# Kernel optimization log

Measured on AMD Instinct MI355X. Metric: run time of the kernel, lower is better.

The kernel has to match this reference:

```python
import jax, jax.numpy as jnp
import numpy as np

DIM = 4096
NH = 32       # query heads
NKV = 8       # kv heads
HD = DIM // NH  # 128
B = 1
S = 2048
ROPE_BASE = 10000.0


def rope_tables(seq_len, head_dim, base=ROPE_BASE):
    inv_freq = 1.0 / base ** (jnp.arange(0, head_dim, 2, dtype=jnp.float32) / head_dim)
    t = jnp.arange(seq_len, dtype=jnp.float32)
    freqs = jnp.einsum('i,j->ij', t, inv_freq)          # [S, HD/2]
    emb = jnp.concatenate([freqs, freqs], axis=-1)      # [S, HD]
    return jnp.cos(emb), jnp.sin(emb)


def apply_rope(x, cos, sin):
    # x: [B, H, S, HD]; matches torch apply_rotary_emb (chunk halves)
    x1, x2 = jnp.split(x, 2, axis=-1)
    d = x1.shape[-1]
    c = cos[None, None, :, :d]
    s = sin[None, None, :, :d]
    return jnp.concatenate([x1 * c - x2 * s, x2 * c + x1 * s], axis=-1)


def setup_inputs() -> dict:
    key = jax.random.key(0)
    k0, k1, k2, k3, k4 = jax.random.split(key, 5)
    sc = 0.02  # typical init scale for stable softmax
    return {
        'x': jax.random.normal(k0, (B, S, DIM), jnp.float32),
        'wq': jax.random.normal(k1, (DIM, NH * HD), jnp.float32) * sc,
        'wk': jax.random.normal(k2, (DIM, NKV * HD), jnp.float32) * sc,
        'wv': jax.random.normal(k3, (DIM, NKV * HD), jnp.float32) * sc,
        'wo': jax.random.normal(k4, (NH * HD, DIM), jnp.float32) * sc,
        'mask': jnp.ones((1,), jnp.bool_),  # presence triggers is_causal=True in torch SDPA path
    }


def reference(x, wq, wk, wv, wo, mask):
    Bsz, Sl, _ = x.shape
    n_rep = NH // NKV
    q = (x @ wq).reshape(Bsz, Sl, NH, HD).transpose(0, 2, 1, 3)    # [B,NH,S,HD]
    k = (x @ wk).reshape(Bsz, Sl, NKV, HD).transpose(0, 2, 1, 3)   # [B,NKV,S,HD]
    v = (x @ wv).reshape(Bsz, Sl, NKV, HD).transpose(0, 2, 1, 3)
    cos, sin = rope_tables(Sl, HD)
    q = apply_rope(q, cos, sin)
    k = apply_rope(k, cos, sin)
    # GQA without repeat_interleave: group query heads per kv head
    qg = q.reshape(Bsz, NKV, n_rep, Sl, HD)
    scale = HD ** -0.5
    scores = jnp.einsum('bgrqd,bgkd->bgrqk', qg, k) * scale        # [B,NKV,n_rep,S,S]
    causal = jnp.tril(jnp.ones((Sl, Sl), dtype=bool))
    scores = jnp.where(causal[None, None, None], scores, jnp.finfo(scores.dtype).min)
    attn = jax.nn.softmax(scores, axis=-1)
    out = jnp.einsum('bgrqk,bgkd->bgrqd', attn, v)                 # [B,NKV,n_rep,S,HD]
    out = out.reshape(Bsz, NH, Sl, HD).transpose(0, 2, 1, 3).reshape(Bsz, Sl, NH * HD)
    return out @ wo
```

## Files before the change

kernel.cpp:

```cpp
#include <hip/hip_runtime.h>
#include <hip/hip_bf16.h>
#include <cstdint>
#include <cmath>

#define DIM 4096
#define NH 32
#define NKV 8
#define HD 128
#define S_LEN 2048
#define KVD (NKV * HD)
#define QS 6144
#define SCALE 0.08838834764831845f

typedef __attribute__((ext_vector_type(4))) float f32x4;
typedef __attribute__((ext_vector_type(8))) short short8;

__device__ __forceinline__ short f2bf(float f) {
  union { float f; uint32_t u; } v; v.f = f;
  uint32_t u = v.u;
  u += 0x7fffu + ((u >> 16) & 1u);
  return (short)(u >> 16);
}
__device__ __forceinline__ float bf2f(short b) {
  union { uint32_t u; float f; } v; v.u = ((uint32_t)(uint16_t)b) << 16;
  return v.f;
}

__device__ __forceinline__ void async16(const void* g, void* l) {
  __builtin_amdgcn_global_load_lds(
      (__attribute__((address_space(1))) void*)(g),
      (__attribute__((address_space(3))) void*)(l), 16, 0, 0);
}


__global__ void rope_tables_k(float* __restrict__ ct, float* __restrict__ st) {
  const int i = blockIdx.x * blockDim.x + threadIdx.x;
  if (i >= S_LEN * 64) return;
  const int s = i >> 6, d = i & 63;
  const float inv = powf(10000.0f, -(float)(2 * d) / 128.0f);
  const float fr = (float)s * inv;
  ct[i] = cosf(fr);
  st[i] = sinf(fr);
}

__global__ void cast_f32_bf16_k(const float* __restrict__ in, short* __restrict__ out, int n4) {
  const int i = blockIdx.x * blockDim.x + threadIdx.x;
  if (i >= n4) return;
  const float4 v = ((const float4*)in)[i];
  short4 o;
  o.x = f2bf(v.x); o.y = f2bf(v.y); o.z = f2bf(v.z); o.w = f2bf(v.w);
  ((short4*)out)[i] = o;
}

__global__ void transpose_cast_k(const float* __restrict__ wsrc, short* __restrict__ wt,
                                 int K, int N) {
  __shared__ float tile[32][33];
  const int tx = threadIdx.x, ty = threadIdx.y;
  const int c0 = blockIdx.x * 32, r0 = blockIdx.y * 32;
#pragma unroll
  for (int j = 0; j < 4; ++j)
    tile[ty + j * 8][tx] = wsrc[(size_t)(r0 + ty + j * 8) * N + c0 + tx];
  __syncthreads();
#pragma unroll
  for (int j = 0; j < 4; ++j)
    wt[(size_t)(c0 + ty + j * 8) * K + r0 + tx] = f2bf(tile[tx][ty + j * 8]);
}

__global__ void transpose_bf16_k(const short* __restrict__ in, short* __restrict__ out,
                                 int R, int C, int ldi) {
  __shared__ short tile[32][33];
  const int tx = threadIdx.x, ty = threadIdx.y;
  const int c0 = blockIdx.x * 32, r0 = blockIdx.y * 32;
#pragma unroll
  for (int j = 0; j < 4; ++j)
    tile[ty + j * 8][tx] = in[(size_t)(r0 + ty + j * 8) * ldi + c0 + tx];
  __syncthreads();
#pragma unroll
  for (int j = 0; j < 4; ++j)
    out[(size_t)(c0 + ty + j * 8) * R + r0 + tx] = tile[tx][ty + j * 8];
}

__global__ void rope_apply_k(short* __restrict__ xq, int ld, const float* __restrict__ ct,
                             const float* __restrict__ st, int nheads) {
  const int i = blockIdx.x * blockDim.x + threadIdx.x;
  const int total = S_LEN * nheads * 64;
  if (i >= total) return;
  const int d = i & 63;
  const int t = i >> 6;
  const int hh = t % nheads;
  const int s = t / nheads;
  short* p = xq + (size_t)s * ld + hh * HD + d;
  const float x1 = bf2f(p[0]);
  const float x2 = bf2f(p[64]);
  const float c = ct[(s << 6) + d];
  const float sn = st[(s << 6) + d];
  p[0]  = f2bf(x1 * c - x2 * sn);
  p[64] = f2bf(x2 * c + x1 * sn);
}


#define PH3_SYNC(VM)                                             \
  asm volatile("s_waitcnt vmcnt(" #VM ")" ::: "memory");         \
  __builtin_amdgcn_s_barrier();                                  \
  asm volatile("s_waitcnt lgkmcnt(0)" ::: "memory");             \
  __builtin_amdgcn_sched_barrier(0);                             \
  __builtin_amdgcn_s_setprio(1)

#define PH3_END()                                                \
  __builtin_amdgcn_s_setprio(0);                                 \
  __builtin_amdgcn_sched_barrier(0);                             \
  __builtin_amdgcn_s_barrier()

__global__ __launch_bounds__(512, 2) void gemm192_k(
    const short* __restrict__ A, const short* __restrict__ BT,
    short* __restrict__ C, int M, int N, int K) {
  __shared__ __attribute__((aligned(16))) short ldsA[2][256 * 64];
  __shared__ __attribute__((aligned(16))) short ldsB[2][192 * 64];
  const int tid = threadIdx.x;
  const int l = tid & 63, w = tid >> 6;
  const int wrM = w >> 1, wcN = w & 1;
  const int lrow = l & 15, lg = l >> 4;
  const int cofs[2] = {(lg ^ (lrow & 7)) << 3, ((4 + lg) ^ (lrow & 7)) << 3};
  (void)M;

  int bid = blockIdx.x;
  const int cpx = gridDim.x >> 3;
  bid = (bid & 7) * cpx + (bid >> 3);
  const int ntn = N / 192;
  const int m0 = (bid / ntn) << 8;
  const int n0 = (bid % ntn) * 192;

  auto stage = [&](int tau) {
    const int k0 = tau << 6;
    short* bd = &ldsB[tau & 1][0];
    short* ad = &ldsA[tau & 1][0];
#pragma unroll
    for (int it = 0; it < 3; ++it) {
      const int e = it * 512 + tid;
      const int row = e >> 3;
      const int js = (e & 7) ^ (row & 7);
      async16(BT + (size_t)(n0 + row) * K + k0 + js * 8, bd + e * 8);
    }
#pragma unroll
    for (int it = 0; it < 4; ++it) {
      const int e = it * 512 + tid;
      const int row = e >> 3;
      const int js = (e & 7) ^ (row & 7);
      async16(A + (size_t)(m0 + row) * K + k0 + js * 8, ad + e * 8);
    }
  };
  auto rdA = [&](short8 (&dst)[4][2], int b) {
    const short* p = &ldsA[b][0];
#pragma unroll
    for (int mi = 0; mi < 4; ++mi) {
      const int row = wrM * 64 + mi * 16 + lrow;
#pragma unroll
      for (int kk = 0; kk < 2; ++kk)
        dst[mi][kk] = *(const short8*)(p + row * 64 + cofs[kk]);
    }
  };
  auto rdB = [&](short8 (&dst)[2][2], int b, int pr) {
    const short* p = &ldsB[b][0];
#pragma unroll
    for (int ni = 0; ni < 2; ++ni) {
      const int row = wcN * 96 + pr * 32 + ni * 16 + lrow;
#pragma unroll
      for (int kk = 0; kk < 2; ++kk)
        dst[ni][kk] = *(const short8*)(p + row * 64 + cofs[kk]);
    }
  };

  f32x4 acc[4][6] = {};
  auto third = [&](short8 (&Af)[4][2], int pr, short8 (&Bf)[2][2]) {
#pragma unroll
    for (int kk = 0; kk < 2; ++kk)
#pragma unroll
      for (int mi = 0; mi < 4; ++mi)
#pragma unroll
        for (int ni = 0; ni < 2; ++ni)
          acc[mi][pr * 2 + ni] = __builtin_amdgcn_mfma_f32_16x16x32_bf16(
              Af[mi][kk], Bf[ni][kk], acc[mi][pr * 2 + ni], 0, 0, 0);
  };

  short8 Aa[4][2], Ab[4][2], B0f[2][2], B1f[2][2], B2f[2][2];

  stage(0); stage(1);
  asm volatile("s_waitcnt vmcnt(7)" ::: "memory");
  __builtin_amdgcn_s_barrier();
  rdB(B0f, 0, 0);
  rdA(Aa, 0);

  const int KT = K >> 6;
  for (int u = 0; u < (KT - 2) / 2; ++u) {
    const int e = 2 * u;
    rdB(B1f, 0, 1); rdB(B2f, 0, 2);
    PH3_SYNC(7);  third(Aa, 0, B0f); PH3_END();
    stage(e + 2);
    PH3_SYNC(7);  third(Aa, 1, B1f); PH3_END();
    rdB(B0f, 1, 0); rdA(Ab, 1);
    PH3_SYNC(7);  third(Aa, 2, B2f); PH3_END();
    rdB(B1f, 1, 1); rdB(B2f, 1, 2);
    PH3_SYNC(7);  third(Ab, 0, B0f); PH3_END();
    stage(e + 3);
    PH3_SYNC(7);  third(Ab, 1, B1f); PH3_END();
    rdB(B0f, 0, 0); rdA(Aa, 0);
    PH3_SYNC(7);  third(Ab, 2, B2f); PH3_END();
  }
  rdB(B1f, 0, 1); rdB(B2f, 0, 2);
  PH3_SYNC(7);  third(Aa, 0, B0f); PH3_END();
  PH3_SYNC(0);  third(Aa, 1, B1f); PH3_END();
  rdB(B0f, 1, 0); rdA(Ab, 1);
  PH3_SYNC(0);  third(Aa, 2, B2f); PH3_END();
  rdB(B1f, 1, 1); rdB(B2f, 1, 2);
  PH3_SYNC(0);  third(Ab, 0, B0f); PH3_END();
  PH3_SYNC(0);  third(Ab, 1, B1f); PH3_END();
  PH3_SYNC(0);  third(Ab, 2, B2f); PH3_END();

  const int orow0 = m0 + wrM * 64 + lg * 4;
  const int ocol0 = n0 + wcN * 96 + lrow;
#pragma unroll
  for (int mi = 0; mi < 4; ++mi)
#pragma unroll
    for (int n = 0; n < 6; ++n)
#pragma unroll
      for (int r = 0; r < 4; ++r)
        C[(size_t)(orow0 + mi * 16 + r) * N + (ocol0 + n * 16)] = f2bf(acc[mi][n][r]);
}


template <int BM, int NBUF, int OUT_BF16>
__global__ __launch_bounds__(512, 2) void gemm_p(
    const short* __restrict__ A, const short* __restrict__ BT,
    void* __restrict__ Cv, int M, int N, int K) {
  constexpr int TILE = (BM + 256) * 64;
  constexpr int LA = BM / 64;
  constexpr int NP = BM / 64;
  __shared__ __attribute__((aligned(16))) short lds[NBUF][TILE];

  const int tid = threadIdx.x;
  const int w = tid >> 6, l = tid & 63;
  const int wr = w >> 2, wc = w & 3;
  const int lrow = l & 15, lg = l >> 4;

  int bid = blockIdx.x;
  const int cpx = gridDim.x >> 3;
  bid = (bid & 7) * cpx + (bid >> 3);
  const int ntn = N >> 8;
  const int m0 = (bid / ntn) * BM;
  const int n0 = (bid % ntn) << 8;

  auto stage = [&](int kt, int buf) {
    const int k0 = kt << 6;
    short* dst = &lds[buf][0];
#pragma unroll
    for (int it = 0; it < LA; ++it) {
      const int e = it * 512 + tid;
      const int row = e >> 3, j = e & 7;
      const int jsrc = j ^ (row & 7);
      async16(A + (size_t)(m0 + row) * K + k0 + jsrc * 8, dst + e * 8);
    }
#pragma unroll
    for (int it = 0; it < 4; ++it) {
      const int e = it * 512 + tid;
      const int row = e >> 3, j = e & 7;
      const int jsrc = j ^ (row & 7);
      async16(BT + (size_t)(n0 + row) * K + k0 + jsrc * 8, dst + BM * 64 + e * 8);
    }
  };

  auto vwait = [&](int J) {
    if constexpr (BM == 256) {
      if (J >= 1) asm volatile("s_waitcnt vmcnt(8)" ::: "memory");
      else        asm volatile("s_waitcnt vmcnt(0)" ::: "memory");
    } else {
      if (J >= 2)      asm volatile("s_waitcnt vmcnt(12)" ::: "memory");
      else if (J == 1) asm volatile("s_waitcnt vmcnt(6)" ::: "memory");
      else             asm volatile("s_waitcnt vmcnt(0)" ::: "memory");
    }
  };

  f32x4 acc[NP * 2][4] = {};

  const int KT = K >> 6;
#pragma unroll
  for (int t = 0; t < NBUF; ++t) stage(t, t);
  vwait(NBUF - 1);
  __builtin_amdgcn_s_barrier();

  for (int kt = 0; kt < KT; ++kt) {
    const int buf = kt % NBUF;
    const short* Ah = &lds[buf][0];
    const short* Bh = &lds[buf][BM * 64];
    short8 bfrag[2][4];

#pragma unroll
    for (int p = 0; p < NP; ++p) {
      short8 afrag[2][2];
#pragma unroll
      for (int mi = 0; mi < 2; ++mi) {
        const int row = wr * (BM / 2) + (p * 2 + mi) * 16 + lrow;
#pragma unroll
        for (int kk = 0; kk < 2; ++kk)
          afrag[mi][kk] =
              *(const short8*)(Ah + row * 64 + (((kk * 4 + lg) ^ (row & 7)) << 3));
      }
      if (p == 0) {
#pragma unroll
        for (int n = 0; n < 4; ++n) {
          const int row = wc * 64 + n * 16 + lrow;
#pragma unroll
          for (int kk = 0; kk < 2; ++kk)
            bfrag[kk][n] =
                *(const short8*)(Bh + row * 64 + (((kk * 4 + lg) ^ (row & 7)) << 3));
        }
      }
      __builtin_amdgcn_s_barrier();
      asm volatile("s_waitcnt lgkmcnt(0)" ::: "memory");
      __builtin_amdgcn_s_setprio(1);
#pragma unroll
      for (int kk = 0; kk < 2; ++kk)
#pragma unroll
        for (int mi = 0; mi < 2; ++mi)
#pragma unroll
          for (int n = 0; n < 4; ++n)
            acc[p * 2 + mi][n] = __builtin_amdgcn_mfma_f32_16x16x32_bf16(
                afrag[mi][kk], bfrag[kk][n], acc[p * 2 + mi][n], 0, 0, 0);
      __builtin_amdgcn_s_setprio(0);
      __builtin_amdgcn_s_barrier();
    }
    if (kt + 1 < KT) {
      const int nst = kt + NBUF;
      if (nst < KT) stage(nst, buf);
      const int J = (nst < KT ? nst : KT - 1) - (kt + 1);
      vwait(J);
      __builtin_amdgcn_s_barrier();
    }
  }

  const int orow0 = m0 + wr * (BM / 2) + lg * 4;
  const int ocol0 = n0 + wc * 64 + lrow;
#pragma unroll
  for (int m = 0; m < NP * 2; ++m)
#pragma unroll
    for (int n = 0; n < 4; ++n)
#pragma unroll
      for (int r = 0; r < 4; ++r) {
        const size_t idx = (size_t)(orow0 + m * 16 + r) * N + (ocol0 + n * 16);
        if (OUT_BF16)
          ((short*)Cv)[idx] = f2bf(acc[m][n][r]);
        else
          ((float*)Cv)[idx] = acc[m][n][r];
      }
}


__global__ __launch_bounds__(256, 3) void attn_k(
    const short* __restrict__ Q, const short* __restrict__ Kc,
    const short* __restrict__ VTg, short* __restrict__ O) {
  __shared__ __attribute__((aligned(16))) short Ks[2][64 * 128];
  __shared__ __attribute__((aligned(16))) short Vt[2][128 * 64];
  __shared__ __attribute__((aligned(16))) short Ps[4][32 * 64];

  const int tid = threadIdx.x;
  const int w = tid >> 6, l = tid & 63;
  const int lrow = l & 15, lg = l >> 4;

  int b = blockIdx.x, h, qt;
  if (b < 256) { h = b >> 3; qt = 15 - (b & 7); }
  else { b -= 256; h = b >> 3; qt = b & 7; }
  const int kvh = h >> 2;
  const int qb0 = qt * 128;
  const int qrow0 = qb0 + w * 32;
  const int nkt = 2 * qt + 2;

  short8 qf[2][4];
#pragma unroll
  for (int nq = 0; nq < 2; ++nq) {
    const short* qp = Q + (size_t)(qrow0 + nq * 16 + lrow) * QS + h * HD;
#pragma unroll
    for (int c = 0; c < 4; ++c) qf[nq][c] = *(const short8*)(qp + c * 32 + lg * 8);
  }

  f32x4 o_acc[2][8] = {};
  float m[2] = {-INFINITY, -INFINITY};
  float lsum[2] = {0.f, 0.f};

  auto stage = [&](int kb, int buf) {
    short* kd = Ks[buf];
    short* vd = Vt[buf];
#pragma unroll
    for (int it = 0; it < 4; ++it) {
      const int e = it * 256 + tid;
      const int row = e >> 4, j = e & 15;
      const int jsrc = (j & 8) | ((j ^ row) & 7);
      async16(Kc + (size_t)(kb + row) * QS + kvh * HD + jsrc * 8, kd + e * 8);
    }
#pragma unroll
    for (int it = 0; it < 4; ++it) {
      const int e = it * 256 + tid;
      const int d = e >> 3, j = e & 7;
      const int jsrc = (j ^ d) & 7;
      async16(VTg + (size_t)(kvh * HD + d) * S_LEN + kb + jsrc * 8, vd + e * 8);
    }
  };

  stage(0, 0);
  int cur = 0;

  for (int kt = 0; kt < nkt; ++kt) {
    __syncthreads();
    if (kt + 1 < nkt) stage((kt + 1) * 64, cur ^ 1);
    const int kb = kt * 64;

    if (kb <= qrow0 + 31) {
      const char* ks = (const char*)Ks[cur];
      const char* vt = (const char*)Vt[cur];
      char* psb = (char*)Ps[w];

      f32x4 stq[4][2] = {};
#pragma unroll
      for (int c = 0; c < 4; ++c) {
#pragma unroll
        for (int mk = 0; mk < 4; ++mk) {
          const short8 kf = *(const short8*)(
              ks + (mk * 16 + lrow) * 256 + (((c * 4 + lg) ^ (lrow & 7)) << 4));
          stq[mk][0] = __builtin_amdgcn_mfma_f32_16x16x32_bf16(kf, qf[0][c], stq[mk][0], 0, 0, 0);
          stq[mk][1] = __builtin_amdgcn_mfma_f32_16x16x32_bf16(kf, qf[1][c], stq[mk][1], 0, 0, 0);
        }
      }

      const bool needmask = (kb + 63 > qrow0);
#pragma unroll
      for (int mk = 0; mk < 4; ++mk)
#pragma unroll
        for (int nq = 0; nq < 2; ++nq)
#pragma unroll
          for (int r = 0; r < 4; ++r) {
            float v = stq[mk][nq][r] * SCALE;
            if (needmask && (kb + mk * 16 + lg * 4 + r > qrow0 + nq * 16 + lrow))
              v = -INFINITY;
            stq[mk][nq][r] = v;
          }

      float vmax[2];
#pragma unroll
      for (int nq = 0; nq < 2; ++nq) {
        float v = stq[0][nq][0];
#pragma unroll
        for (int mk = 0; mk < 4; ++mk)
#pragma unroll
          for (int r = 0; r < 4; ++r) v = fmaxf(v, stq[mk][nq][r]);
        v = fmaxf(v, __shfl_xor(v, 16));
        v = fmaxf(v, __shfl_xor(v, 32));
        vmax[nq] = v;
      }

      const int small = (vmax[0] <= m[0] + 8.0f) && (vmax[1] <= m[1] + 8.0f);
      if (!__all(small)) {
        float al[2];
#pragma unroll
        for (int nq = 0; nq < 2; ++nq) {
          const float mn = fmaxf(m[nq], vmax[nq]);
          al[nq] = __expf(m[nq] - mn);
          m[nq] = mn;
          lsum[nq] *= al[nq];
        }
#pragma unroll
        for (int mmq = 0; mmq < 2; ++mmq)
#pragma unroll
          for (int r = 0; r < 4; ++r) {
            const float a = __shfl(al[mmq], lg * 4 + r);
#pragma unroll
            for (int d = 0; d < 8; ++d) o_acc[mmq][d][r] *= a;
          }
      }

      float rs[2] = {0.f, 0.f};
#pragma unroll
      for (int nq = 0; nq < 2; ++nq) {
#pragma unroll
        for (int mk = 0; mk < 4; ++mk) {
          const float p0 = __expf(stq[mk][nq][0] - m[nq]);
          const float p1 = __expf(stq[mk][nq][1] - m[nq]);
          const float p2 = __expf(stq[mk][nq][2] - m[nq]);
          const float p3 = __expf(stq[mk][nq][3] - m[nq]);
          rs[nq] += (p0 + p1) + (p2 + p3);
          __hip_bfloat16 b0 = __float2bfloat16(p0), b1 = __float2bfloat16(p1);
          __hip_bfloat16 b2 = __float2bfloat16(p2), b3 = __float2bfloat16(p3);
          short4 pk;
          pk.x = *(short*)&b0; pk.y = *(short*)&b1; pk.z = *(short*)&b2; pk.w = *(short*)&b3;
          const int q = nq * 16 + lrow;
          *(short4*)(psb + q * 128 + ((mk * 32 + lg * 8) ^ ((q & 7) << 4))) = pk;
        }
        float r2 = rs[nq];
        r2 += __shfl_xor(r2, 16);
        r2 += __shfl_xor(r2, 32);
        lsum[nq] += r2;
      }

#pragma unroll
      for (int cc = 0; cc < 2; ++cc) {
        const int chunk = ((cc * 4 + lg) ^ (lrow & 7)) << 4;
        const short8 pa0 = *(const short8*)(psb + lrow * 128 + chunk);
        const short8 pa1 = *(const short8*)(psb + (16 + lrow) * 128 + chunk);
#pragma unroll
        for (int d = 0; d < 8; ++d) {
          const short8 vf = *(const short8*)(vt + (d * 16 + lrow) * 128 + chunk);
          o_acc[0][d] = __builtin_amdgcn_mfma_f32_16x16x32_bf16(pa0, vf, o_acc[0][d], 0, 0, 0);
          o_acc[1][d] = __builtin_amdgcn_mfma_f32_16x16x32_bf16(pa1, vf, o_acc[1][d], 0, 0, 0);
        }
      }
    }
    cur ^= 1;
  }

  float linv[2] = {1.0f / lsum[0], 1.0f / lsum[1]};
#pragma unroll
  for (int mmq = 0; mmq < 2; ++mmq)
#pragma unroll
    for (int r = 0; r < 4; ++r) {
      const float li = __shfl(linv[mmq], lg * 4 + r);
      short* op = O + (size_t)(qrow0 + mmq * 16 + lg * 4 + r) * DIM + h * HD;
#pragma unroll
      for (int d = 0; d < 8; ++d)
        op[d * 16 + lrow] = f2bf(o_acc[mmq][d][r] * li);
    }
}


extern "C" void kernel_launch(void* const* d_in, const int* in_sizes, int n_in,
                              void* d_out, int out_size, void* d_ws, size_t ws_size,
                              hipStream_t stream) {
  const float* x  = (const float*)d_in[0];
  const float* wq = (const float*)d_in[1];
  const float* wk = (const float*)d_in[2];
  const float* wv = (const float*)d_in[3];
  const float* wo = (const float*)d_in[4];
  float* out = (float*)d_out;
  (void)in_sizes; (void)n_in; (void)out_size; (void)ws_size;

  char* ws = (char*)d_ws;
  size_t off = 0;
  auto alloc = [&](size_t bytes) -> void* {
    void* p = ws + off;
    off += (bytes + 255) & ~(size_t)255;
    return p;
  };
  short* xb     = (short*)alloc((size_t)S_LEN * DIM * 2);
  short* wqkvT  = (short*)alloc((size_t)QS * DIM * 2);
  short* woT    = (short*)alloc((size_t)DIM * DIM * 2);
  short* qkv    = (short*)alloc((size_t)S_LEN * QS * 2);
  short* vtg    = (short*)alloc((size_t)KVD * S_LEN * 2);
  short* ao     = (short*)alloc((size_t)S_LEN * DIM * 2);
  float* ct     = (float*)alloc((size_t)S_LEN * 64 * 4);
  float* st     = (float*)alloc((size_t)S_LEN * 64 * 4);

  rope_tables_k<<<(S_LEN * 64) / 256, 256, 0, stream>>>(ct, st);
  cast_f32_bf16_k<<<(S_LEN * DIM / 4) / 256, 256, 0, stream>>>(x, xb, S_LEN * DIM / 4);
  transpose_cast_k<<<dim3(DIM / 32, DIM / 32), dim3(32, 8), 0, stream>>>(wq, wqkvT, DIM, DIM);
  transpose_cast_k<<<dim3(KVD / 32, DIM / 32), dim3(32, 8), 0, stream>>>(
      wk, wqkvT + (size_t)4096 * DIM, DIM, KVD);
  transpose_cast_k<<<dim3(KVD / 32, DIM / 32), dim3(32, 8), 0, stream>>>(
      wv, wqkvT + (size_t)5120 * DIM, DIM, KVD);
  transpose_cast_k<<<dim3(DIM / 32, DIM / 32), dim3(32, 8), 0, stream>>>(wo, woT, DIM, DIM);

  gemm192_k<<<dim3((S_LEN / 256) * (QS / 192)), 512, 0, stream>>>(
      xb, wqkvT, qkv, S_LEN, QS, DIM);

  rope_apply_k<<<(S_LEN * 40 * 64) / 256, 256, 0, stream>>>(qkv, QS, ct, st, 40);

  transpose_bf16_k<<<dim3(KVD / 32, S_LEN / 32), dim3(32, 8), 0, stream>>>(
      qkv + 5120, vtg, S_LEN, KVD, QS);

  attn_k<<<dim3(512), 256, 0, stream>>>(qkv, qkv + 4096, vtg, ao);

  gemm_p<128, 3, 0><<<dim3((S_LEN / 128) * (DIM / 256)), 512, 0, stream>>>(
      ao, woT, out, S_LEN, DIM, DIM);
}
```

Measured before the change: 354.1 us.

## Rewrite output GEMM with double-buffered register-prefetch pipeline and partial lgkm waits

Replaces the generic triple-buffered gemm_p for the output projection with a dedicated double-buffered kernel. It prefetches A and B fragments into registers ahead of the MFMA phases, splits each k-tile into two halves, and issues global staging inside barrier-protected phases. In the QKV GEMM it also relaxes the lgkmcnt waits to partial counts and moves the stage calls inside the synced phases. The aim is to overlap LDS reads and global loads with MFMA work and cut stall time, at the cost of more register pressure and subtle wait-count correctness requirements.

```diff
diff --git a/kernel.cpp b/kernel.cpp
--- a/kernel.cpp
+++ b/kernel.cpp
@@ -98,18 +98,18 @@
   p[64] = f2bf(x2 * c + x1 * sn);
 }
 
-
-#define PH3_SYNC(VM)                                             \
+#define SYNC2(VM, LG)                                            \
   asm volatile("s_waitcnt vmcnt(" #VM ")" ::: "memory");         \
   __builtin_amdgcn_s_barrier();                                  \
-  asm volatile("s_waitcnt lgkmcnt(0)" ::: "memory");             \
+  asm volatile("s_waitcnt lgkmcnt(" #LG ")" ::: "memory");       \
   __builtin_amdgcn_sched_barrier(0);                             \
   __builtin_amdgcn_s_setprio(1)
 
-#define PH3_END()                                                \
+#define PH_END()                                                 \
   __builtin_amdgcn_s_setprio(0);                                 \
   __builtin_amdgcn_sched_barrier(0);                             \
   __builtin_amdgcn_s_barrier()
+
 
 __global__ __launch_bounds__(512, 2) void gemm192_k(
     const short* __restrict__ A, const short* __restrict__ BT,
@@ -194,27 +194,25 @@
   for (int u = 0; u < (KT - 2) / 2; ++u) {
     const int e = 2 * u;
     rdB(B1f, 0, 1); rdB(B2f, 0, 2);
-    PH3_SYNC(7);  third(Aa, 0, B0f); PH3_END();
-    stage(e + 2);
-    PH3_SYNC(7);  third(Aa, 1, B1f); PH3_END();
+    SYNC2(7, 8);  third(Aa, 0, B0f); PH_END();
+    SYNC2(0, 0);  stage(e + 2); third(Aa, 1, B1f); PH_END();
     rdB(B0f, 1, 0); rdA(Ab, 1);
-    PH3_SYNC(7);  third(Aa, 2, B2f); PH3_END();
+    SYNC2(7, 12); third(Aa, 2, B2f); PH_END();
     rdB(B1f, 1, 1); rdB(B2f, 1, 2);
-    PH3_SYNC(7);  third(Ab, 0, B0f); PH3_END();
-    stage(e + 3);
-    PH3_SYNC(7);  third(Ab, 1, B1f); PH3_END();
+    SYNC2(7, 8);  third(Ab, 0, B0f); PH_END();
+    SYNC2(0, 0);  stage(e + 3); third(Ab, 1, B1f); PH_END();
     rdB(B0f, 0, 0); rdA(Aa, 0);
-    PH3_SYNC(7);  third(Ab, 2, B2f); PH3_END();
+    SYNC2(7, 12); third(Ab, 2, B2f); PH_END();
   }
   rdB(B1f, 0, 1); rdB(B2f, 0, 2);
-  PH3_SYNC(7);  third(Aa, 0, B0f); PH3_END();
-  PH3_SYNC(0);  third(Aa, 1, B1f); PH3_END();
+  SYNC2(7, 8);  third(Aa, 0, B0f); PH_END();
+  SYNC2(0, 0);  third(Aa, 1, B1f); PH_END();
   rdB(B0f, 1, 0); rdA(Ab, 1);
-  PH3_SYNC(0);  third(Aa, 2, B2f); PH3_END();
+  SYNC2(0, 12); third(Aa, 2, B2f); PH_END();
   rdB(B1f, 1, 1); rdB(B2f, 1, 2);
-  PH3_SYNC(0);  third(Ab, 0, B0f); PH3_END();
-  PH3_SYNC(0);  third(Ab, 1, B1f); PH3_END();
-  PH3_SYNC(0);  third(Ab, 2, B2f); PH3_END();
+  SYNC2(0, 8);  third(Ab, 0, B0f); PH_END();
+  SYNC2(0, 0);  third(Ab, 1, B1f); PH_END();
+  SYNC2(0, 0);  third(Ab, 2, B2f); PH_END();
 
   const int orow0 = m0 + wrM * 64 + lg * 4;
   const int ocol0 = n0 + wcN * 96 + lrow;
@@ -228,129 +226,113 @@
 }
 
 
-template <int BM, int NBUF, int OUT_BF16>
-__global__ __launch_bounds__(512, 2) void gemm_p(
+__global__ __launch_bounds__(512, 2) void gemm_wo2_k(
     const short* __restrict__ A, const short* __restrict__ BT,
-    void* __restrict__ Cv, int M, int N, int K) {
-  constexpr int TILE = (BM + 256) * 64;
-  constexpr int LA = BM / 64;
-  constexpr int NP = BM / 64;
-  __shared__ __attribute__((aligned(16))) short lds[NBUF][TILE];
-
+    float* __restrict__ C, int M, int N, int K) {
+  __shared__ __attribute__((aligned(16))) short ldsA[2][128 * 64];
+  __shared__ __attribute__((aligned(16))) short ldsB[2][256 * 64];
   const int tid = threadIdx.x;
-  const int w = tid >> 6, l = tid & 63;
-  const int wr = w >> 2, wc = w & 3;
+  const int l = tid & 63, w = tid >> 6;
+  const int wrM = w >> 2, wcN = w & 3;
   const int lrow = l & 15, lg = l >> 4;
+  const int cofs[2] = {(lg ^ (lrow & 7)) << 3, ((4 + lg) ^ (lrow & 7)) << 3};
+  (void)M;
 
   int bid = blockIdx.x;
   const int cpx = gridDim.x >> 3;
   bid = (bid & 7) * cpx + (bid >> 3);
   const int ntn = N >> 8;
-  const int m0 = (bid / ntn) * BM;
+  const int m0 = (bid / ntn) << 7;
   const int n0 = (bid % ntn) << 8;
 
-  auto stage = [&](int kt, int buf) {
-    const int k0 = kt << 6;
-    short* dst = &lds[buf][0];
-#pragma unroll
-    for (int it = 0; it < LA; ++it) {
+  auto stage = [&](int tau) {
+    const int k0 = tau << 6;
+    short* ad = &ldsA[tau & 1][0];
+    short* bd = &ldsB[tau & 1][0];
+#pragma unroll
+    for (int it = 0; it < 2; ++it) {
       const int e = it * 512 + tid;
-      const int row = e >> 3, j = e & 7;
-      const int jsrc = j ^ (row & 7);
-      async16(A + (size_t)(m0 + row) * K + k0 + jsrc * 8, dst + e * 8);
+      const int row = e >> 3;
+      const int js = (e & 7) ^ (row & 7);
+      async16(A + (size_t)(m0 + row) * K + k0 + js * 8, ad + e * 8);
     }
 #pragma unroll
     for (int it = 0; it < 4; ++it) {
       const int e = it * 512 + tid;
-      const int row = e >> 3, j = e & 7;
-      const int jsrc = j ^ (row & 7);
-      async16(BT + (size_t)(n0 + row) * K + k0 + jsrc * 8, dst + BM * 64 + e * 8);
-    }
-  };
-
-  auto vwait = [&](int J) {
-    if constexpr (BM == 256) {
-      if (J >= 1) asm volatile("s_waitcnt vmcnt(8)" ::: "memory");
-      else        asm volatile("s_waitcnt vmcnt(0)" ::: "memory");
-    } else {
-      if (J >= 2)      asm volatile("s_waitcnt vmcnt(12)" ::: "memory");
-      else if (J == 1) asm volatile("s_waitcnt vmcnt(6)" ::: "memory");
-      else             asm volatile("s_waitcnt vmcnt(0)" ::: "memory");
-    }
-  };
-
-  f32x4 acc[NP * 2][4] = {};
+      const int row = e >> 3;
+      const int js = (e & 7) ^ (row & 7);
+      async16(BT + (size_t)(n0 + row) * K + k0 + js * 8, bd + e * 8);
+    }
+  };
+  auto rdA = [&](short8 (&dst)[4][2], int b) {
+    const short* p = &ldsA[b][0];
+#pragma unroll
+    for (int mi = 0; mi < 4; ++mi) {
+      const int row = wrM * 64 + mi * 16 + lrow;
+#pragma unroll
+      for (int kk = 0; kk < 2; ++kk)
+        dst[mi][kk] = *(const short8*)(p + row * 64 + cofs[kk]);
+    }
+  };
+  auto rdB = [&](short8 (&dst)[2][2], int b, int h) {
+    const short* p = &ldsB[b][0];
+#pragma unroll
+    for (int ni = 0; ni < 2; ++ni) {
+      const int row = wcN * 64 + h * 32 + ni * 16 + lrow;
+#pragma unroll
+      for (int kk = 0; kk < 2; ++kk)
+        dst[ni][kk] = *(const short8*)(p + row * 64 + cofs[kk]);
+    }
+  };
+
+  f32x4 acc[4][4] = {};
+  auto half = [&](short8 (&Af)[4][2], int h, short8 (&Bf)[2][2]) {
+#pragma unroll
+    for (int kk = 0; kk < 2; ++kk)
+#pragma unroll
+      for (int mi = 0; mi < 4; ++mi)
+#pragma unroll
+        for (int ni = 0; ni < 2; ++ni)
+          acc[mi][h * 2 + ni] = __builtin_amdgcn_mfma_f32_16x16x32_bf16(
+              Af[mi][kk], Bf[ni][kk], acc[mi][h * 2 + ni], 0, 0, 0);
+  };
+
+  short8 Aa[4][2], Ab[4][2], H0[2][2], H1[2][2];
+
+  stage(0); stage(1);
+  asm volatile("s_waitcnt vmcnt(6)" ::: "memory");
+  __builtin_amdgcn_s_barrier();
+  rdA(Aa, 0); rdB(H0, 0, 0);
 
   const int KT = K >> 6;
-#pragma unroll
-  for (int t = 0; t < NBUF; ++t) stage(t, t);
-  vwait(NBUF - 1);
-  __builtin_amdgcn_s_barrier();
-
-  for (int kt = 0; kt < KT; ++kt) {
-    const int buf = kt % NBUF;
-    const short* Ah = &lds[buf][0];
-    const short* Bh = &lds[buf][BM * 64];
-    short8 bfrag[2][4];
-
-#pragma unroll
-    for (int p = 0; p < NP; ++p) {
-      short8 afrag[2][2];
-#pragma unroll
-      for (int mi = 0; mi < 2; ++mi) {
-        const int row = wr * (BM / 2) + (p * 2 + mi) * 16 + lrow;
-#pragma unroll
-        for (int kk = 0; kk < 2; ++kk)
-          afrag[mi][kk] =
-              *(const short8*)(Ah + row * 64 + (((kk * 4 + lg) ^ (row & 7)) << 3));
-      }
-      if (p == 0) {
-#pragma unroll
-        for (int n = 0; n < 4; ++n) {
-          const int row = wc * 64 + n * 16 + lrow;
-#pragma unroll
-          for (int kk = 0; kk < 2; ++kk)
-            bfrag[kk][n] =
-                *(const short8*)(Bh + row * 64 + (((kk * 4 + lg) ^ (row & 7)) << 3));
-        }
-      }
-      __builtin_amdgcn_s_barrier();
-      asm volatile("s_waitcnt lgkmcnt(0)" ::: "memory");
-      __builtin_amdgcn_s_setprio(1);
-#pragma unroll
-      for (int kk = 0; kk < 2; ++kk)
-#pragma unroll
-        for (int mi = 0; mi < 2; ++mi)
-#pragma unroll
-          for (int n = 0; n < 4; ++n)
-            acc[p * 2 + mi][n] = __builtin_amdgcn_mfma_f32_16x16x32_bf16(
-                afrag[mi][kk], bfrag[kk][n], acc[p * 2 + mi][n], 0, 0, 0);
-      __builtin_amdgcn_s_setprio(0);
-      __builtin_amdgcn_s_barrier();
-    }
-    if (kt + 1 < KT) {
-      const int nst = kt + NBUF;
-      if (nst < KT) stage(nst, buf);
-      const int J = (nst < KT ? nst : KT - 1) - (kt + 1);
-      vwait(J);
-      __builtin_amdgcn_s_barrier();
-    }
+  for (int u = 0; u < (KT - 2) / 2; ++u) {
+    const int e = 2 * u;
+    rdB(H1, 0, 1);
+    SYNC2(6, 4);  half(Aa, 0, H0); PH_END();
+    SYNC2(0, 0);  stage(e + 2); rdA(Ab, 1); rdB(H0, 1, 0);
+                  half(Aa, 1, H1); PH_END();
+    rdB(H1, 1, 1);
+    SYNC2(6, 4);  half(Ab, 0, H0); PH_END();
+    SYNC2(0, 0);  stage(e + 3); rdA(Aa, 0); rdB(H0, 0, 0);
+                  half(Ab, 1, H1); PH_END();
   }
-
-  const int orow0 = m0 + wr * (BM / 2) + lg * 4;
-  const int ocol0 = n0 + wc * 64 + lrow;
-#pragma unroll
-  for (int m = 0; m < NP * 2; ++m)
+  rdB(H1, 0, 1);
+  SYNC2(6, 4);  half(Aa, 0, H0); PH_END();
+  SYNC2(0, 0);  rdA(Ab, 1); rdB(H0, 1, 0);
+                half(Aa, 1, H1); PH_END();
+  rdB(H1, 1, 1);
+  SYNC2(0, 4);  half(Ab, 0, H0); PH_END();
+  SYNC2(0, 0);  half(Ab, 1, H1); PH_END();
+
+  const int orow0 = m0 + wrM * 64 + lg * 4;
+  const int ocol0 = n0 + wcN * 64 + lrow;
+#pragma unroll
+  for (int mi = 0; mi < 4; ++mi)
 #pragma unroll
     for (int n = 0; n < 4; ++n)
 #pragma unroll
-      for (int r = 0; r < 4; ++r) {
-        const size_t idx = (size_t)(orow0 + m * 16 + r) * N + (ocol0 + n * 16);
-        if (OUT_BF16)
-          ((short*)Cv)[idx] = f2bf(acc[m][n][r]);
-        else
-          ((float*)Cv)[idx] = acc[m][n][r];
-      }
+      for (int r = 0; r < 4; ++r)
+        C[(size_t)(orow0 + mi * 16 + r) * N + (ocol0 + n * 16)] = acc[mi][n][r];
 }
 
 
@@ -574,6 +556,6 @@
 
   attn_k<<<dim3(512), 256, 0, stream>>>(qkv, qkv + 4096, vtg, ao);
 
-  gemm_p<128, 3, 0><<<dim3((S_LEN / 128) * (DIM / 256)), 512, 0, stream>>>(
+  gemm_wo2_k<<<dim3((S_LEN / 128) * (DIM / 256)), 512, 0, stream>>>(
       ao, woT, out, S_LEN, DIM, DIM);
 }
```

After: 343.6 us. 3.0% less time.
